# Kernel optimization log

Measured on AMD Instinct MI355X. Metric: run time of the kernel, lower is better.

The kernel has to match this reference:

```python
import jax, jax.numpy as jnp
import numpy as np

K = 7
G = 16
PAD = K // 2
EPS = 1e-5


def setup_inputs() -> dict:
    key = jax.random.key(0)
    ks = jax.random.split(key, 8)
    C = 256
    Cr = C // 4  # ratio=4 bottleneck
    inputs = jax.random.normal(ks[0], (4, C, 56, 56), dtype=jnp.float32)
    W1 = jax.random.normal(ks[1], (Cr, C), dtype=jnp.float32) * 0.05
    b1 = jax.random.normal(ks[2], (Cr,), dtype=jnp.float32) * 0.05
    gamma = jax.random.normal(ks[3], (Cr,), dtype=jnp.float32) * 0.1 + 1.0
    beta = jax.random.normal(ks[4], (Cr,), dtype=jnp.float32) * 0.1
    mean = jax.random.normal(ks[5], (Cr,), dtype=jnp.float32) * 0.1
    var = jax.random.uniform(ks[6], (Cr,), dtype=jnp.float32) * 0.5 + 0.5
    W2 = jax.random.normal(ks[7], (G * K * K, Cr), dtype=jnp.float32) * 0.05
    b2 = jnp.zeros((G * K * K,), dtype=jnp.float32)
    return {"inputs": inputs, "W1": W1, "b1": b1, "gamma": gamma,
            "beta": beta, "mean": mean, "var": var, "W2": W2, "b2": b2}


def reference(inputs, W1, b1, gamma, beta, mean, var, W2, b2):
    B, C, H, W = inputs.shape
    Cg = C // G
    # kernel-generation branch: 1x1 conv -> BN (eval stats) -> relu -> 1x1 conv
    t = jnp.einsum('bchw,oc->bohw', inputs, W1) + b1[None, :, None, None]
    scale = gamma / jnp.sqrt(var + EPS)
    t = t * scale[None, :, None, None] + (beta - mean * scale)[None, :, None, None]
    t = jax.nn.relu(t)
    w = jnp.einsum('bchw,oc->bohw', t, W2) + b2[None, :, None, None]
    w = w.reshape(B, G, K * K, H, W)  # per-pixel kernel
    # involution: accumulate shifted slices instead of materializing unfold
    xp = jnp.pad(inputs, ((0, 0), (0, 0), (PAD, PAD), (PAD, PAD)))
    xg = xp.reshape(B, G, Cg, H + 2 * PAD, W + 2 * PAD)
    out = jnp.zeros((B, G, Cg, H, W), dtype=inputs.dtype)
    k = 0
    for i in range(K):
        for j in range(K):
            out = out + xg[:, :, :, i:i + H, j:j + W] * w[:, :, k][:, :, None, :, :]
            k += 1
    return out.reshape(B, C, H, W)
```

## Files before the change

kernel.cpp:

```cpp
#include <hip/hip_runtime.h>

#define HW    3136
#define HDIM  56
#define CIN   256
#define CR    64
#define NG    16
#define KK    49
#define BEPS  1e-5f

#define RB     2
#define NBAND  28
#define CHALF  28
#define WSTR   60
#define XR     8
#define XC     36
#define XCG    16
#define XTOT   (XR * XCG * XC)
#define NSLOT  1152
#define K1X    (HW / 16)
#define K1PREP 32

typedef __attribute__((ext_vector_type(8))) short short8;
typedef __attribute__((ext_vector_type(4))) float f32x4;

__device__ __forceinline__ unsigned short f2bf(float f) {
    union { float f; unsigned u; } v; v.f = f;
    unsigned r = (v.u + 0x7FFFu + ((v.u >> 16) & 1u)) >> 16;
    return (unsigned short)r;
}

__device__ __forceinline__ void gload_lds16(const float* gp, float* lp) {
    __builtin_amdgcn_global_load_lds(
        (const __attribute__((address_space(1))) void*)gp,
        (__attribute__((address_space(3))) void*)lp, 16, 0, 0);
}

__global__ __launch_bounds__(128) void k1_gemm(
    const float* __restrict__ x, const float* __restrict__ W1,
    const float* __restrict__ b1, const float* __restrict__ gamma,
    const float* __restrict__ beta, const float* __restrict__ mean,
    const float* __restrict__ var, const float* __restrict__ W2,
    unsigned short* __restrict__ t_bf, unsigned short* __restrict__ W2bT)
{
    const int tid = threadIdx.x;
    const int b = blockIdx.y;

    if (blockIdx.x >= K1X) {
        if (b) return;
        int i = (blockIdx.x - K1X) * 128 + tid;
#pragma unroll
        for (int r = 0; r < 16; r++) {
            int j = r * 4096 + i;
            int c = j & 63, tap = (j >> 6) & 63, g = j >> 12;
            float v = (tap < KK) ? W2[((size_t)g * KK + tap) * CR + c] : 0.f;
            W2bT[j] = f2bf(v);
        }
        return;
    }

    __shared__ float red[64 * 17];

    const int lane = tid & 63, l15 = lane & 15, q = lane >> 4;
    const int wid = tid >> 6;
    const int pxb = blockIdx.x * 16;
    const int kb = wid * 128;

    const float* xp = x + (size_t)b * CIN * HW + pxb + l15;

    float sc[4], bias[4];
#pragma unroll
    for (int nt = 0; nt < 4; nt++) {
        int o = 16 * nt + l15;
        float s = gamma[o] * rsqrtf(var[o] + BEPS);
        sc[nt] = s;
        bias[nt] = b1[o] * s + beta[o] - mean[o] * s;
    }

    f32x4 acc[4];
#pragma unroll
    for (int nt = 0; nt < 4; nt++) acc[nt] = (f32x4){0.f, 0.f, 0.f, 0.f};

#pragma unroll
    for (int kc = 0; kc < 4; kc++) {
        short8 af;
#pragma unroll
        for (int j = 0; j < 8; j++)
            af[j] = (short)f2bf(xp[(size_t)(kb + kc * 32 + q * 8 + j) * HW]);
#pragma unroll
        for (int nt = 0; nt < 4; nt++) {
            const float* wp = &W1[(size_t)(16 * nt + l15) * CIN + kb + kc * 32 + q * 8];
            float4 wa = *(const float4*)wp;
            float4 wb = *(const float4*)(wp + 4);
            short8 bf;
            bf[0] = (short)f2bf(wa.x * sc[nt]); bf[1] = (short)f2bf(wa.y * sc[nt]);
            bf[2] = (short)f2bf(wa.z * sc[nt]); bf[3] = (short)f2bf(wa.w * sc[nt]);
            bf[4] = (short)f2bf(wb.x * sc[nt]); bf[5] = (short)f2bf(wb.y * sc[nt]);
            bf[6] = (short)f2bf(wb.z * sc[nt]); bf[7] = (short)f2bf(wb.w * sc[nt]);
            acc[nt] = __builtin_amdgcn_mfma_f32_16x16x32_bf16(af, bf, acc[nt], 0, 0, 0);
        }
    }

    if (wid == 1) {
#pragma unroll
        for (int nt = 0; nt < 4; nt++)
#pragma unroll
            for (int r = 0; r < 4; r++)
                red[lane * 17 + nt * 4 + r] = acc[nt][r];
    }
    __syncthreads();
    if (wid == 0) {
#pragma unroll
        for (int nt = 0; nt < 4; nt++) {
#pragma unroll
            for (int r = 0; r < 4; r++) {
                int px = pxb + 4 * q + r;
                float v = acc[nt][r] + red[lane * 17 + nt * 4 + r] + bias[nt];
                t_bf[((size_t)b * HW + px) * CR + 16 * nt + l15] = f2bf(fmaxf(v, 0.f));
            }
        }
    }
}

__global__ __launch_bounds__(256, 5) void k2_fused(
    const float* __restrict__ x, const unsigned short* __restrict__ t_bf,
    const unsigned short* __restrict__ W2bT, const float* __restrict__ b2,
    float* __restrict__ out)
{
    __shared__ float w_lds[KK * WSTR];
    __shared__ float x_lds[XTOT];

    const int tid = threadIdx.x;

    const int p    = blockIdx.x + 56 * blockIdx.y + 896 * blockIdx.z;
    const int ord  = (p & 7) * 448 + (p >> 3);
    const int band = ord % 28;
    const int chalf = (ord / 28) & 1;
    const int g    = (ord / 56) & 15;
    const int b    = ord / 896;

    const int h0 = band * RB, c0 = chalf * CHALF;
    const int lane = tid & 63, l15 = lane & 15, q = lane >> 4;
    const int wid = tid >> 6;

#pragma unroll
    for (int k = 0; k < 5; k++) {
        int i = wid + 4 * k;
        if (i < 18)
            *(float4*)&x_lds[(i * 64 + lane) * 4] = make_float4(0.f, 0.f, 0.f, 0.f);
    }
    asm volatile("s_waitcnt lgkmcnt(0)" ::: "memory");

    short8 bfr[4][2];
#pragma unroll
    for (int nt = 0; nt < 4; nt++)
#pragma unroll
        for (int ks = 0; ks < 2; ks++)
            bfr[nt][ks] = *(const short8*)&W2bT[((size_t)g * 64 + 16 * nt + l15) * 64 + ks * 32 + q * 8];

    const int arow = wid >> 1, aseg = wid & 1;
    int apx = (h0 + arow) * HDIM + c0 + aseg * 16 + l15;
    if (apx > HW - 1) apx = HW - 1;
    const unsigned short* tp = &t_bf[((size_t)b * HW + apx) * CR];
    short8 a0 = *(const short8*)&tp[q * 8];
    short8 a1 = *(const short8*)&tp[32 + q * 8];

    float b2v[4];
#pragma unroll
    for (int nt = 0; nt < 4; nt++) {
        int tap = 16 * nt + l15;
        b2v[nt] = (tap < KK) ? b2[g * KK + tap] : 0.f;
    }

#pragma unroll
    for (int k = 0; k < 5; k++) {
        int i = wid + 4 * k;
        if (i < 18) {
            int slot = i * 64 + lane;
            int s = slot % 9, rc = slot / 9;
            int cg = rc & 15, rowx = rc >> 4;
            int hy = h0 - 3 + rowx, gx = c0 + 4 * s - 4;
            if (hy >= 0 && hy < HDIM && gx >= 0 && gx <= HDIM - 4)
                gload_lds16(&x[((size_t)b * CIN + g * 16 + cg) * HW + hy * HDIM + gx],
                            &x_lds[i * 256]);
        }
    }

    {
        const int cl = aseg * 16 + 4 * q;
#pragma unroll
        for (int nt = 0; nt < 4; nt++) {
            f32x4 acc = (f32x4){0.f, 0.f, 0.f, 0.f};
            acc = __builtin_amdgcn_mfma_f32_16x16x32_bf16(a0, bfr[nt][0], acc, 0, 0, 0);
            acc = __builtin_amdgcn_mfma_f32_16x16x32_bf16(a1, bfr[nt][1], acc, 0, 0, 0);
            int tap = 16 * nt + l15;
            if (tap < KK && cl < CHALF) {
                *(float4*)&w_lds[tap * WSTR + arow * CHALF + cl] =
                    make_float4(acc[0] + b2v[nt], acc[1] + b2v[nt],
                                acc[2] + b2v[nt], acc[3] + b2v[nt]);
            }
        }
    }
    __syncthreads();

    if (tid < 224) {
        const int cg   = tid & 15;
        const int rq   = tid >> 4;
        const int row  = rq & 1;
        const int quad = rq >> 1;
        const int colb = quad * 4, h = h0 + row;

        float acc[4] = {0.f, 0.f, 0.f, 0.f};

#pragma unroll
        for (int di = 0; di < 7; di++) {
            float wv[7][4];
#pragma unroll
            for (int dj = 0; dj < 7; dj++) {
                float4 wq = *(const float4*)&w_lds[(di * 7 + dj) * WSTR + row * CHALF + colb];
                wv[dj][0] = wq.x; wv[dj][1] = wq.y; wv[dj][2] = wq.z; wv[dj][3] = wq.w;
            }
            const float* xr = &x_lds[((row + di) * 16 + cg) * XC + colb];
            float4 A  = *(const float4*)&xr[0];
            float4 Bv = *(const float4*)&xr[4];
            float4 Cv = *(const float4*)&xr[8];
            float win[12] = {A.x, A.y, A.z, A.w, Bv.x, Bv.y, Bv.z, Bv.w,
                             Cv.x, Cv.y, Cv.z, Cv.w};
#pragma unroll
            for (int dj = 0; dj < 7; dj++)
#pragma unroll
                for (int kk = 0; kk < 4; kk++)
                    acc[kk] += win[kk + dj + 1] * wv[dj][kk];
        }
        float* op = &out[((size_t)b * CIN + g * 16 + cg) * HW + h * HDIM + c0 + colb];
        *(float4*)op = make_float4(acc[0], acc[1], acc[2], acc[3]);
    }
}

extern "C" void kernel_launch(void* const* d_in, const int* in_sizes, int n_in,
                              void* d_out, int out_size, void* d_ws, size_t ws_size,
                              hipStream_t stream) {
    const float* x     = (const float*)d_in[0];
    const float* W1    = (const float*)d_in[1];
    const float* b1    = (const float*)d_in[2];
    const float* gamma = (const float*)d_in[3];
    const float* beta  = (const float*)d_in[4];
    const float* mean  = (const float*)d_in[5];
    const float* var   = (const float*)d_in[6];
    const float* W2    = (const float*)d_in[7];
    const float* b2    = (const float*)d_in[8];
    float* out = (float*)d_out;

    unsigned short* t_bf = (unsigned short*)d_ws;
    unsigned short* W2bT = t_bf + (size_t)4 * HW * CR;

    dim3 g1(K1X + K1PREP, 4);
    k1_gemm<<<g1, 128, 0, stream>>>(x, W1, b1, gamma, beta, mean, var, W2,
                                    t_bf, W2bT);

    dim3 g2(NBAND * 2, NG, 4);
    k2_fused<<<g2, 256, 0, stream>>>(x, t_bf, W2bT, b2, out);
}
```

Measured before the change: 114.7 us.

## Widen k1 split-K to four waves and register-block channels in involution stage

k1 now runs 256 threads per block, with four waves each covering 64 input channels, reducing through a larger LDS buffer. The W2 prep blocks are resized to match. In k2, the involution phase moves from 224 threads with one channel each to 56 threads with four channels each, so each thread reuses its loaded per-pixel weights across four channels and cuts LDS weight reads. The catch is far fewer active threads in that phase and higher register pressure, which is why k2's occupancy hint drops from 5 to 4.

Measured after the change: 130.5 us. 1.14x slower.

```diff
diff --git a/kernel.cpp b/kernel.cpp
--- a/kernel.cpp
+++ b/kernel.cpp
@@ -16,9 +16,8 @@
 #define XC     36
 #define XCG    16
 #define XTOT   (XR * XCG * XC)
-#define NSLOT  1152
 #define K1X    (HW / 16)
-#define K1PREP 32
+#define K1PREP 8
 
 typedef __attribute__((ext_vector_type(8))) short short8;
 typedef __attribute__((ext_vector_type(4))) float f32x4;
@@ -35,7 +34,7 @@
         (__attribute__((address_space(3))) void*)lp, 16, 0, 0);
 }
 
-__global__ __launch_bounds__(128) void k1_gemm(
+__global__ __launch_bounds__(256) void k1_gemm(
     const float* __restrict__ x, const float* __restrict__ W1,
     const float* __restrict__ b1, const float* __restrict__ gamma,
     const float* __restrict__ beta, const float* __restrict__ mean,
@@ -47,10 +46,10 @@
 
     if (blockIdx.x >= K1X) {
         if (b) return;
-        int i = (blockIdx.x - K1X) * 128 + tid;
-#pragma unroll
-        for (int r = 0; r < 16; r++) {
-            int j = r * 4096 + i;
+        int i = (blockIdx.x - K1X) * 256 + tid;
+#pragma unroll
+        for (int r = 0; r < 32; r++) {
+            int j = r * 2048 + i;
             int c = j & 63, tap = (j >> 6) & 63, g = j >> 12;
             float v = (tap < KK) ? W2[((size_t)g * KK + tap) * CR + c] : 0.f;
             W2bT[j] = f2bf(v);
@@ -58,12 +57,12 @@
         return;
     }
 
-    __shared__ float red[64 * 17];
+    __shared__ float red[3 * 64 * 17];
 
     const int lane = tid & 63, l15 = lane & 15, q = lane >> 4;
     const int wid = tid >> 6;
     const int pxb = blockIdx.x * 16;
-    const int kb = wid * 128;
+    const int kb = wid * 64;
 
     const float* xp = x + (size_t)b * CIN * HW + pxb + l15;
 
@@ -81,7 +80,7 @@
     for (int nt = 0; nt < 4; nt++) acc[nt] = (f32x4){0.f, 0.f, 0.f, 0.f};
 
 #pragma unroll
-    for (int kc = 0; kc < 4; kc++) {
+    for (int kc = 0; kc < 2; kc++) {
         short8 af;
 #pragma unroll
         for (int j = 0; j < 8; j++)
@@ -100,12 +99,12 @@
         }
     }
 
-    if (wid == 1) {
+    if (wid) {
 #pragma unroll
         for (int nt = 0; nt < 4; nt++)
 #pragma unroll
             for (int r = 0; r < 4; r++)
-                red[lane * 17 + nt * 4 + r] = acc[nt][r];
+                red[((wid - 1) * 64 + lane) * 17 + nt * 4 + r] = acc[nt][r];
     }
     __syncthreads();
     if (wid == 0) {
@@ -114,14 +113,18 @@
 #pragma unroll
             for (int r = 0; r < 4; r++) {
                 int px = pxb + 4 * q + r;
-                float v = acc[nt][r] + red[lane * 17 + nt * 4 + r] + bias[nt];
+                float v = acc[nt][r]
+                        + red[(lane) * 17 + nt * 4 + r]
+                        + red[(64 + lane) * 17 + nt * 4 + r]
+                        + red[(128 + lane) * 17 + nt * 4 + r]
+                        + bias[nt];
                 t_bf[((size_t)b * HW + px) * CR + 16 * nt + l15] = f2bf(fmaxf(v, 0.f));
             }
         }
     }
 }
 
-__global__ __launch_bounds__(256, 5) void k2_fused(
+__global__ __launch_bounds__(256, 4) void k2_fused(
     const float* __restrict__ x, const unsigned short* __restrict__ t_bf,
     const unsigned short* __restrict__ W2bT, const float* __restrict__ b2,
     float* __restrict__ out)
@@ -202,14 +205,17 @@
     }
     __syncthreads();
 
-    if (tid < 224) {
-        const int cg   = tid & 15;
-        const int rq   = tid >> 4;
-        const int row  = rq & 1;
-        const int quad = rq >> 1;
+    if (tid < 56) {
+        const int cgq  = tid & 3;
+        const int row  = (tid >> 2) & 1;
+        const int quad = tid >> 3;
         const int colb = quad * 4, h = h0 + row;
 
-        float acc[4] = {0.f, 0.f, 0.f, 0.f};
+        float acc[4][4];
+#pragma unroll
+        for (int e = 0; e < 4; e++)
+#pragma unroll
+            for (int kk = 0; kk < 4; kk++) acc[e][kk] = 0.f;
 
 #pragma unroll
         for (int di = 0; di < 7; di++) {
@@ -219,20 +225,26 @@
                 float4 wq = *(const float4*)&w_lds[(di * 7 + dj) * WSTR + row * CHALF + colb];
                 wv[dj][0] = wq.x; wv[dj][1] = wq.y; wv[dj][2] = wq.z; wv[dj][3] = wq.w;
             }
-            const float* xr = &x_lds[((row + di) * 16 + cg) * XC + colb];
-            float4 A  = *(const float4*)&xr[0];
-            float4 Bv = *(const float4*)&xr[4];
-            float4 Cv = *(const float4*)&xr[8];
-            float win[12] = {A.x, A.y, A.z, A.w, Bv.x, Bv.y, Bv.z, Bv.w,
-                             Cv.x, Cv.y, Cv.z, Cv.w};
-#pragma unroll
-            for (int dj = 0; dj < 7; dj++)
-#pragma unroll
-                for (int kk = 0; kk < 4; kk++)
-                    acc[kk] += win[kk + dj + 1] * wv[dj][kk];
-        }
-        float* op = &out[((size_t)b * CIN + g * 16 + cg) * HW + h * HDIM + c0 + colb];
-        *(float4*)op = make_float4(acc[0], acc[1], acc[2], acc[3]);
+#pragma unroll
+            for (int e = 0; e < 4; e++) {
+                const float* xr = &x_lds[((row + di) * 16 + 4 * cgq + e) * XC + colb];
+                float4 A  = *(const float4*)&xr[0];
+                float4 Bv = *(const float4*)&xr[4];
+                float4 Cv = *(const float4*)&xr[8];
+                float win[12] = {A.x, A.y, A.z, A.w, Bv.x, Bv.y, Bv.z, Bv.w,
+                                 Cv.x, Cv.y, Cv.z, Cv.w};
+#pragma unroll
+                for (int dj = 0; dj < 7; dj++)
+#pragma unroll
+                    for (int kk = 0; kk < 4; kk++)
+                        acc[e][kk] += win[kk + dj + 1] * wv[dj][kk];
+            }
+        }
+#pragma unroll
+        for (int e = 0; e < 4; e++) {
+            float* op = &out[((size_t)b * CIN + g * 16 + 4 * cgq + e) * HW + h * HDIM + c0 + colb];
+            *(float4*)op = make_float4(acc[e][0], acc[e][1], acc[e][2], acc[e][3]);
+        }
     }
 }
 
@@ -254,7 +266,7 @@
     unsigned short* W2bT = t_bf + (size_t)4 * HW * CR;
 
     dim3 g1(K1X + K1PREP, 4);
-    k1_gemm<<<g1, 128, 0, stream>>>(x, W1, b1, gamma, beta, mean, var, W2,
+    k1_gemm<<<g1, 256, 0, stream>>>(x, W1, b1, gamma, beta, mean, var, W2,
                                     t_bf, W2bT);
 
     dim3 g2(NBAND * 2, NG, 4);
```
